# Performance work log

Measured on AMD Instinct MI355X. Metric: run time of the kernel, lower is better.

## Reference

```python
import jax, jax.numpy as jnp
import numpy as np

HEADS = 16
DIM_HEAD = 64
MASK_VALUE = -(np.finfo(np.float32).max / 2)


def setup_inputs() -> dict:
    key = jax.random.key(0)
    k1, k2, k3 = jax.random.split(key, 3)
    B, N, D = 2, 2048, 1024
    inner = HEADS * DIM_HEAD
    x = jax.random.normal(k1, (B, N, D), dtype=jnp.float32)
    w_qkv = jax.random.normal(k2, (D, 3 * inner), dtype=jnp.float32) * (D ** -0.5)
    w_out = jax.random.normal(k3, (inner, D), dtype=jnp.float32) * (inner ** -0.5)
    b_out = jnp.zeros((D,), dtype=jnp.float32)
    return {"x": x, "w_qkv": w_qkv, "w_out": w_out, "b_out": b_out}


def reference(x, w_qkv, w_out, b_out):
    B, N, D = x.shape
    H, Dh = HEADS, DIM_HEAD
    qkv = x @ w_qkv                                   # [B, N, 3*H*Dh]
    q, k, v = jnp.split(qkv, 3, axis=-1)
    # [B, N, H*Dh] -> [B, H, N, Dh]
    split_heads = lambda t: t.reshape(B, N, H, Dh).transpose(0, 2, 1, 3)
    q, k, v = split_heads(q), split_heads(k), split_heads(v)
    scale = Dh ** -0.5
    sim = jnp.einsum('bhid,bhjd->bhij', q, k) * scale  # [B, H, N, N]
    # causal additive mask: MASK_VALUE above the diagonal
    causal = jnp.triu(jnp.ones((N, N), dtype=bool), k=1)
    mask = jnp.where(causal, jnp.float32(MASK_VALUE), 0.0)
    sim = sim + mask[None, None, :, :]
    attn = jax.nn.softmax(sim, axis=-1)
    out = jnp.einsum('bhij,bhjd->bhid', attn, v)       # [B, H, N, Dh]
    out = out.transpose(0, 2, 1, 3).reshape(B, N, H * Dh)
    return out @ w_out + b_out
```

## Files before the change

kernel.cpp:

```cpp
#include <hip/hip_runtime.h>
#include <hip/hip_bf16.h>

typedef __attribute__((ext_vector_type(4)))  float    f32x4;
typedef __attribute__((ext_vector_type(16))) float    f32x16;
typedef __attribute__((ext_vector_type(8)))  short    bf16x8;
typedef __attribute__((ext_vector_type(4)))  short    s16x4;
typedef __attribute__((ext_vector_type(4)))  unsigned u32x4;

#define B_    2
#define N_    2048
#define D_    1024
#define HEADS 16
#define DH    64
#define M_    4096
#define INNER 1024

static __device__ __forceinline__ short f2bf(float f) {
    __hip_bfloat16 h = __float2bfloat16(f);
    return __builtin_bit_cast(short, h);
}
static __device__ __forceinline__ float bf2f(short s) {
    unsigned u = ((unsigned)(unsigned short)s) << 16;
    return __builtin_bit_cast(float, u);
}
static __device__ __forceinline__ unsigned pack2(float lo, float hi) {
    return ((unsigned)(unsigned short)f2bf(lo)) |
           (((unsigned)(unsigned short)f2bf(hi)) << 16);
}
static __device__ __forceinline__ unsigned cvtpk(float lo, float hi) {
    unsigned r;
    asm("v_cvt_pk_bf16_f32 %0, %1, %2" : "=v"(r) : "v"(lo), "v"(hi));
    return r;
}
static __device__ __forceinline__ void plswap(unsigned& a, unsigned& b) {
    asm("v_permlane32_swap_b32 %0, %1" : "+v"(a), "+v"(b));
}
static __device__ __forceinline__ float fexp2(float x) {
    float r;
    asm("v_exp_f32 %0, %1" : "=v"(r) : "v"(x));
    return r;
}
static __device__ __forceinline__ float flog2(float x) {
    float r;
    asm("v_log_f32 %0, %1" : "=v"(r) : "v"(x));
    return r;
}
static __device__ __forceinline__ float vmax16(f32x16 v) {
    float a = fmaxf(fmaxf(v[0], v[1]), fmaxf(v[2], v[3]));
    float b = fmaxf(fmaxf(v[4], v[5]), fmaxf(v[6], v[7]));
    float c = fmaxf(fmaxf(v[8], v[9]), fmaxf(v[10], v[11]));
    float d = fmaxf(fmaxf(v[12], v[13]), fmaxf(v[14], v[15]));
    return fmaxf(fmaxf(a, b), fmaxf(c, d));
}
static __device__ __forceinline__ float vsum16(f32x16 v) {
    float a = (v[0] + v[1]) + (v[2] + v[3]);
    float b = (v[4] + v[5]) + (v[6] + v[7]);
    float c = (v[8] + v[9]) + (v[10] + v[11]);
    float d = (v[12] + v[13]) + (v[14] + v[15]);
    return (a + b) + (c + d);
}

static __device__ __forceinline__ void transpose_tile(const float* __restrict__ in,
                                                      short* __restrict__ out,
                                                      int R, int C, int bx32, int by32,
                                                      float* t ) {
    int tx = threadIdx.x & 31, ty = threadIdx.x >> 5;
    int bx = bx32 * 32, by = by32 * 32;
#pragma unroll
    for (int j = 0; j < 32; j += 8)
        t[(ty + j) * 33 + tx] = in[(long)(by + ty + j) * C + bx + tx];
    __syncthreads();
#pragma unroll
    for (int j = 0; j < 32; j += 8)
        out[(long)(bx + ty + j) * R + by + tx] = f2bf(t[tx * 33 + ty + j]);
}

__global__ void __launch_bounds__(256) prep_k(const float* __restrict__ x,
                                              short* __restrict__ xb,
                                              const float* __restrict__ w_qkv,
                                              short* __restrict__ wqkvT,
                                              const float* __restrict__ w_out,
                                              short* __restrict__ woutT) {
    __shared__ float t[32 * 33];
    int bid = blockIdx.x;
    if (bid < 4096) {
        int i = bid * 256 + threadIdx.x;
        f32x4 v = ((const f32x4*)x)[i];
        s16x4 o;
        o[0] = f2bf(v[0]); o[1] = f2bf(v[1]); o[2] = f2bf(v[2]); o[3] = f2bf(v[3]);
        ((s16x4*)xb)[i] = o;
    } else if (bid < 4096 + 3072) {
        int tt = bid - 4096;
        transpose_tile(w_qkv, wqkvT, 1024, 3072, tt % 96, tt / 96, t);
    } else {
        int tt = bid - 7168;
        transpose_tile(w_out, woutT, 1024, 1024, tt % 32, tt / 32, t);
    }
}

template <int ROWS>
static __device__ __forceinline__ void stage_swz(const short* __restrict__ src,
                                                 int ldElems, short* lds, int tid) {
    constexpr int CH = (ROWS * 128) / (256 * 16);
#pragma unroll
    for (int c = 0; c < CH; ++c) {
        int o   = (tid + c * 256) * 16;
        int row = o >> 7;
        int kb  = (o & 127) ^ ((row & 7) << 4);
        const char* g = (const char*)src + (long)row * ldElems * 2 + kb;
        __builtin_amdgcn_global_load_lds(
            (const __attribute__((address_space(1))) void*)g,
            (__attribute__((address_space(3))) void*)((char*)lds + o), 16, 0, 0);
    }
}
static __device__ __forceinline__ bf16x8 lds_frag(const short* lds, int row, int kbyte) {
    return *(const bf16x8*)((const char*)lds + (row << 7) + (kbyte ^ ((row & 7) << 4)));
}

__global__ void __launch_bounds__(256) gemm_k(const short* __restrict__ A,
                                              const short* __restrict__ Bt, int K,
                                              short* __restrict__ q_out,
                                              short* __restrict__ k_out,
                                              short* __restrict__ v_out) {
    __shared__ __align__(16) short As[128 * 64];
    __shared__ __align__(16) short Bs[128 * 64];
    int tid = threadIdx.x;
    int lane = tid & 63, w = tid >> 6, wr = w >> 1, wc = w & 1;
    int l15 = lane & 15, lg = lane >> 4;
    int nx = gridDim.x;
    int flat = blockIdx.y * nx + blockIdx.x;
    int total = nx * gridDim.y;
    int cpx = total >> 3;
    int swz = (flat & 7) * cpx + (flat >> 3);
    int row0 = (swz / nx) * 128, col0 = (swz % nx) * 128;

    f32x4 acc[4][4] = {};

    for (int k0 = 0; k0 < K; k0 += 64) {
        stage_swz<128>(A + (long)row0 * K + k0, K, As, tid);
        stage_swz<128>(Bt + (long)col0 * K + k0, K, Bs, tid);
        __syncthreads();
#pragma unroll
        for (int kb = 0; kb < 2; ++kb) {
            int kbyte = kb * 64 + (lg << 4);
            bf16x8 af[4], bfr[4];
#pragma unroll
            for (int mr = 0; mr < 4; ++mr)
                af[mr] = lds_frag(As, wr * 64 + mr * 16 + l15, kbyte);
#pragma unroll
            for (int nr = 0; nr < 4; ++nr)
                bfr[nr] = lds_frag(Bs, wc * 64 + nr * 16 + l15, kbyte);
#pragma unroll
            for (int mr = 0; mr < 4; ++mr)
#pragma unroll
                for (int nr = 0; nr < 4; ++nr)
                    acc[mr][nr] = __builtin_amdgcn_mfma_f32_16x16x32_bf16(
                        af[mr], bfr[nr], acc[mr][nr], 0, 0, 0);
        }
        __syncthreads();
    }

#pragma unroll
    for (int mr = 0; mr < 4; ++mr)
#pragma unroll
        for (int nr = 0; nr < 4; ++nr) {
            int gr0 = row0 + wr * 64 + mr * 16 + (lg << 2);
            int gc  = col0 + wc * 64 + nr * 16 + l15;
            int which = gc >> 10, rem = gc & 1023;
            int h = rem >> 6, d = rem & 63;
            int b = gr0 >> 11, nn0 = gr0 & 2047;
            long bh32 = (long)(b * HEADS + h) * 32;
            if (which == 2) {
                int t = nn0 >> 6, ks = (nn0 >> 4) & 3, hb = (nn0 >> 3) & 1;
                long off = (((bh32 + t) * 2 + (d >> 5)) * 4 + ks) * 512
                           + ((hb << 5) + (d & 31)) * 8 + (nn0 & 4);
                s16x4 pk;
#pragma unroll
                for (int reg = 0; reg < 4; ++reg) pk[reg] = f2bf(acc[mr][nr][reg]);
                *(s16x4*)(v_out + off) = pk;
            } else if (which == 1) {
                int dk = d >> 4, hb = (d >> 3) & 1, j = d & 7;
                int t = nn0 >> 6, ss = (nn0 >> 5) & 1;
                long fbase = ((bh32 + t) * 2 + ss) * 4 + dk;
#pragma unroll
                for (int reg = 0; reg < 4; ++reg) {
                    int l31k = (nn0 + reg) & 31;
                    k_out[fbase * 512 + ((hb << 5) + l31k) * 8 + j] =
                        f2bf(acc[mr][nr][reg]);
                }
            } else {
                float sc = 0.180336880f;
#pragma unroll
                for (int reg = 0; reg < 4; ++reg) {
                    int gr = gr0 + reg;
                    int bb = gr >> 11, nn = gr & 2047;
                    q_out[((long)(bb * HEADS + h) * N_ + nn) * DH + d] =
                        f2bf(acc[mr][nr][reg] * sc);
                }
            }
        }
}

__global__ void __launch_bounds__(256) gemm2_k(const short* __restrict__ A,
                                               const short* __restrict__ Bt,
                                               float* __restrict__ f_out,
                                               const float* __restrict__ bias) {
    __shared__ __align__(16) short As[128 * 64];
    __shared__ __align__(16) short Bs[64 * 64];
    int tid = threadIdx.x;
    int lane = tid & 63, w = tid >> 6, wr = w >> 1, wc = w & 1;
    int l15 = lane & 15, lg = lane >> 4;
    const int K = 1024;
    int flat = blockIdx.y * 16 + blockIdx.x;
    int swz = (flat & 7) * 64 + (flat >> 3);
    int row0 = (swz >> 4) * 128, col0 = (swz & 15) * 64;

    f32x4 acc[4][2] = {};

    for (int k0 = 0; k0 < K; k0 += 64) {
        stage_swz<128>(A + (long)row0 * K + k0, K, As, tid);
        stage_swz<64>(Bt + (long)col0 * K + k0, K, Bs, tid);
        __syncthreads();
#pragma unroll
        for (int kb = 0; kb < 2; ++kb) {
            int kbyte = kb * 64 + (lg << 4);
            bf16x8 af[4], bfr[2];
#pragma unroll
            for (int mr = 0; mr < 4; ++mr)
                af[mr] = lds_frag(As, wr * 64 + mr * 16 + l15, kbyte);
#pragma unroll
            for (int nc = 0; nc < 2; ++nc)
                bfr[nc] = lds_frag(Bs, wc * 32 + nc * 16 + l15, kbyte);
#pragma unroll
            for (int mr = 0; mr < 4; ++mr)
#pragma unroll
                for (int nc = 0; nc < 2; ++nc)
                    acc[mr][nc] = __builtin_amdgcn_mfma_f32_16x16x32_bf16(
                        af[mr], bfr[nc], acc[mr][nc], 0, 0, 0);
        }
        __syncthreads();
    }

#pragma unroll
    for (int mr = 0; mr < 4; ++mr)
#pragma unroll
        for (int nc = 0; nc < 2; ++nc) {
            int gc = col0 + wc * 32 + nc * 16 + l15;
            float bv = bias[gc];
#pragma unroll
            for (int reg = 0; reg < 4; ++reg) {
                int gr = row0 + wr * 64 + mr * 16 + (lg << 2) + reg;
                f_out[(long)gr * D_ + gc] = acc[mr][nc][reg] + bv;
            }
        }
}

__global__ void __launch_bounds__(256, 2) attn_k(const short* __restrict__ Qb,
                                                 const short* __restrict__ Kf,
                                                 const short* __restrict__ Vf,
                                                 short* __restrict__ O0,
                                                 short* __restrict__ O1,
                                                 float* __restrict__ lse) {
    __shared__ __align__(16) short Ep[4][2048];
    int tid = threadIdx.x, lane = tid & 63, w = tid >> 6;
    int l31 = lane & 31, hbit = lane >> 5;
    int bq = blockIdx.x;
    int q4 = bq >> 8, rest = bq & 255;
    int bh = rest >> 3, p = rest & 7;
    int x = (q4 < 2) ? (15 - p) : p;
    int seg = q4 & 1;
    int t0 = seg ? (x + 1) : 0;
    int t1 = seg ? (2 * x + 2) : (x + 1);

    const short* Qh = Qb + (long)bh * N_ * DH;
    const short* Kh = Kf + (long)bh * 32 * 4096;
    const short* Vh = Vf + (long)bh * 32 * 4096;
    int lofs = lane * 8;

    int q0 = x * 128 + w * 32;
    int qg = q0 + l31;
    int t1w = min(t1, ((q0 + 31) >> 6) + 1);

    bf16x8 qf[4];
#pragma unroll
    for (int kf = 0; kf < 4; ++kf)
        qf[kf] = *(const bf16x8*)(Qh + (long)qg * DH + kf * 16 + hbit * 8);

    f32x16 o[2] = {};
    float m = -1e30f, l = 0.f;

    for (int t = t0; t < t1w; ++t) {
        const short* kb = Kh + (long)t * 4096;
        const short* vb = Vh + (long)t * 4096;
        int khb = t * 64;

        bf16x8 kfr[2][4];
#pragma unroll
        for (int ss = 0; ss < 2; ++ss)
#pragma unroll
            for (int dk = 0; dk < 4; ++dk)
                kfr[ss][dk] = *(const bf16x8*)(kb + (ss * 4 + dk) * 512 + lofs);

        f32x16 S[2] = {};
        __builtin_amdgcn_s_setprio(1);
#pragma unroll
        for (int ss = 0; ss < 2; ++ss)
#pragma unroll
            for (int dk = 0; dk < 4; ++dk)
                S[ss] = __builtin_amdgcn_mfma_f32_32x32x16_bf16(
                    kfr[ss][dk], qf[dk], S[ss], 0, 0, 0);
        __builtin_amdgcn_s_setprio(0);

        bf16x8 vf[2][4];
#pragma unroll
        for (int df = 0; df < 2; ++df)
#pragma unroll
            for (int ks = 0; ks < 4; ++ks)
                vf[df][ks] = *(const bf16x8*)(vb + (df * 4 + ks) * 512 + lofs);

        if (khb + 63 > q0) {
            int kvl = khb + 4 * hbit;
#pragma unroll
            for (int ss = 0; ss < 2; ++ss)
#pragma unroll
                for (int r = 0; r < 16; ++r) {
                    int kv = kvl + 32 * ss + (r & 3) + 8 * (r >> 2);
                    if (kv > qg) S[ss][r] = -1e30f;
                }
        }

        float pm = fmaxf(vmax16(S[0]), vmax16(S[1]));
        pm = fmaxf(pm, __shfl_xor(pm, 32));
        if (!__all(pm <= m + 8.0f)) {
            float mn = fmaxf(m, pm);
            float corr = fexp2(m - mn);
            m = mn;
            l *= corr;
#pragma unroll
            for (int df = 0; df < 2; ++df)
#pragma unroll
                for (int r = 0; r < 16; ++r) o[df][r] *= corr;
        }
#pragma unroll
        for (int ss = 0; ss < 2; ++ss)
#pragma unroll
            for (int r = 0; r < 16; ++r)
                S[ss][r] = fexp2(S[ss][r] - m);
        l += vsum16(S[0]) + vsum16(S[1]);

        __builtin_amdgcn_s_setprio(1);
#pragma unroll
        for (int ss = 0; ss < 2; ++ss) {
#pragma unroll
            for (int hs = 0; hs < 2; ++hs) {
                unsigned w0 = cvtpk(S[ss][hs * 8 + 0], S[ss][hs * 8 + 1]);
                unsigned w1 = cvtpk(S[ss][hs * 8 + 2], S[ss][hs * 8 + 3]);
                unsigned w2 = cvtpk(S[ss][hs * 8 + 4], S[ss][hs * 8 + 5]);
                unsigned w3 = cvtpk(S[ss][hs * 8 + 6], S[ss][hs * 8 + 7]);
                plswap(w0, w2);
                plswap(w1, w3);
                bf16x8 pfrag = __builtin_bit_cast(bf16x8, (u32x4){w0, w1, w2, w3});
                int ks = ss * 2 + hs;
#pragma unroll
                for (int df = 0; df < 2; ++df)
                    o[df] = __builtin_amdgcn_mfma_f32_32x32x16_bf16(
                        vf[df][ks], pfrag, o[df], 0, 0, 0);
            }
        }
        __builtin_amdgcn_s_setprio(0);
    }

    l += __shfl_xor(l, 32);
    float linv = (l > 0.f) ? 1.0f / l : 0.f;
    if (hbit == 0)
        lse[seg * (32 * N_) + bh * N_ + qg] =
            (l > 0.f) ? (m + flog2(l)) : -__builtin_inff();

    char* Epw = (char*)&Ep[w][0];
#pragma unroll
    for (int df = 0; df < 2; ++df)
#pragma unroll
        for (int r = 0; r < 16; r += 2) {
            unsigned pk = pack2(o[df][r] * linv, o[df][r + 1] * linv);
            int d = df * 32 + (r & 3) + 8 * (r >> 2) + 4 * hbit;
            int cb = d * 2;
            *(unsigned*)(Epw + (l31 << 7) + (cb ^ ((l31 & 7) << 4))) = pk;
        }
    __syncthreads();

    int b = bh >> 4, h = bh & 15;
    int lr = lane >> 1, lc = lane & 1;
    const char* rbase = Epw + (lr << 7);
    long orow = seg ? ((long)(bh * N_ + q0 + lr)) * 64 + lc * 32
                    : ((long)(b * N_ + q0 + lr)) * INNER + h * DH + lc * 32;
    short* dst = seg ? O1 : O0;
#pragma unroll
    for (int j = 0; j < 4; ++j) {
        int cb = lc * 64 + j * 16;
        bf16x8 vv = *(const bf16x8*)(rbase + (cb ^ ((lr & 7) << 4)));
        *(bf16x8*)(dst + orow + j * 8) = vv;
    }
}

__global__ void __launch_bounds__(256) merge_k(short* __restrict__ Ab,
                                               const short* __restrict__ O1,
                                               const float* __restrict__ lse) {
    int gid = blockIdx.x * 256 + threadIdx.x;
    int row = gid >> 3, d0 = (gid & 7) * 8;
    int bh = row >> 11, n = row & 2047;
    float l0 = lse[row];
    float l1 = lse[32 * N_ + row];
    float Mx = fmaxf(l0, l1);
    float w0 = fexp2(l0 - Mx), w1 = fexp2(l1 - Mx);
    float inv = 1.0f / (w0 + w1);
    w0 *= inv; w1 *= inv;
    int b = bh >> 4, h = bh & 15;
    long a_off = ((long)(b * N_ + n) * HEADS + h) * DH + d0;
    long o_off = (long)row * DH + d0;
    bf16x8 v0 = *(const bf16x8*)(Ab + a_off);
    bf16x8 v1 = *(const bf16x8*)(O1 + o_off);
    bf16x8 r;
#pragma unroll
    for (int i = 0; i < 8; ++i)
        r[i] = f2bf(w0 * bf2f(v0[i]) + w1 * bf2f(v1[i]));
    *(bf16x8*)(Ab + a_off) = r;
}


extern "C" void kernel_launch(void* const* d_in, const int* in_sizes, int n_in,
                              void* d_out, int out_size, void* d_ws, size_t ws_size,
                              hipStream_t stream) {
    const float* x     = (const float*)d_in[0];
    const float* w_qkv = (const float*)d_in[1];
    const float* w_out = (const float*)d_in[2];
    const float* b_out = (const float*)d_in[3];
    float* out = (float*)d_out;

    char* ws = (char*)d_ws;
    const size_t MB = 1024 * 1024;
    short* xb    = (short*)(ws + 0 * MB);
    short* wqkvT = (short*)(ws + 8 * MB);
    short* woutT = (short*)(ws + 14 * MB);
    short* Qb    = (short*)(ws + 16 * MB);
    short* Kfb   = (short*)(ws + 24 * MB);
    short* Vfb   = (short*)(ws + 32 * MB);
    short* Ab    = (short*)(ws + 40 * MB);
    short* O1    = (short*)(ws + 0 * MB);
    float* lse   = (float*)(ws + 8 * MB);

    prep_k<<<dim3(4096 + 3072 + 1024), 256, 0, stream>>>(
        x, xb, w_qkv, wqkvT, w_out, woutT);

    gemm_k<<<dim3(3072 / 128, M_ / 128), 256, 0, stream>>>(
        xb, wqkvT, 1024, Qb, Kfb, Vfb);

    attn_k<<<dim3(1024), 256, 0, stream>>>(Qb, Kfb, Vfb, Ab, O1, lse);
    merge_k<<<dim3((32 * N_ * 8) / 256), 256, 0, stream>>>(Ab, O1, lse);

    gemm2_k<<<dim3(1024 / 64, M_ / 128), 256, 0, stream>>>(Ab, woutT, out, b_out);
}
```

Measured before the change: 101.9 us.

## Process 128-key tiles per iteration with per-wave diagonal trimming in attention

The attention loop now walks 128-key tiles instead of 64-key tiles, which halves the number of iterations and softmax/rescale rounds. On the diagonal tile each wave only loads and computes the 32-key sub-blocks it needs (w+1 of them), and the split-KV segments are redefined in terms of the larger tiles. Sched barriers separate the K and V load phases. The cost is more live registers for K/V fragments and S under the 2-blocks-per-CU launch bound, which may cause spills or lower occupancy.

```diff
diff --git a/kernel.cpp b/kernel.cpp
--- a/kernel.cpp
+++ b/kernel.cpp
@@ -269,8 +269,9 @@
     int bh = rest >> 3, p = rest & 7;
     int x = (q4 < 2) ? (15 - p) : p;
     int seg = q4 & 1;
-    int t0 = seg ? (x + 1) : 0;
-    int t1 = seg ? (2 * x + 2) : (x + 1);
+    int sdiv = (x + 2) >> 1;
+    int tA = seg ? sdiv : 0;
+    int tB = seg ? (x + 1) : sdiv;
 
     const short* Qh = Qb + (long)bh * N_ * DH;
     const short* Kh = Kf + (long)bh * 32 * 4096;
@@ -279,7 +280,6 @@
 
     int q0 = x * 128 + w * 32;
     int qg = q0 + l31;
-    int t1w = min(t1, ((q0 + 31) >> 6) + 1);
 
     bf16x8 qf[4];
 #pragma unroll
@@ -287,49 +287,62 @@
         qf[kf] = *(const bf16x8*)(Qh + (long)qg * DH + kf * 16 + hbit * 8);
 
     f32x16 o[2] = {};
+    const f32x16 Zv = {};
     float m = -1e30f, l = 0.f;
 
-    for (int t = t0; t < t1w; ++t) {
-        const short* kb = Kh + (long)t * 4096;
-        const short* vb = Vh + (long)t * 4096;
-        int khb = t * 64;
-
-        bf16x8 kfr[2][4];
-#pragma unroll
-        for (int ss = 0; ss < 2; ++ss)
-#pragma unroll
-            for (int dk = 0; dk < 4; ++dk)
-                kfr[ss][dk] = *(const bf16x8*)(kb + (ss * 4 + dk) * 512 + lofs);
-
-        f32x16 S[2] = {};
+#define VS(df, s16) kv[((df) << 1) + ((s16) >> 2)][(s16) & 3]
+
+    for (int t = tA; t < tB; ++t) {
+        const short* kb = Kh + (long)t * 8192;
+        const short* vb = Vh + (long)t * 8192;
+        bool diag = (t == x);
+        int nss = diag ? (w + 1) : 4;
+
+        bf16x8 kv[4][4];
+#pragma unroll
+        for (int ss = 0; ss < 4; ++ss)
+            if (ss < nss)
+#pragma unroll
+                for (int dk = 0; dk < 4; ++dk)
+                    kv[ss][dk] = *(const bf16x8*)(kb + ss * 2048 + dk * 512 + lofs);
+
+        f32x16 S[4];
         __builtin_amdgcn_s_setprio(1);
 #pragma unroll
-        for (int ss = 0; ss < 2; ++ss)
-#pragma unroll
-            for (int dk = 0; dk < 4; ++dk)
-                S[ss] = __builtin_amdgcn_mfma_f32_32x32x16_bf16(
-                    kfr[ss][dk], qf[dk], S[ss], 0, 0, 0);
+        for (int ss = 0; ss < 4; ++ss)
+            if (ss < nss) {
+                S[ss] = Zv;
+#pragma unroll
+                for (int dk = 0; dk < 4; ++dk)
+                    S[ss] = __builtin_amdgcn_mfma_f32_32x32x16_bf16(
+                        kv[ss][dk], qf[dk], S[ss], 0, 0, 0);
+            }
         __builtin_amdgcn_s_setprio(0);
-
-        bf16x8 vf[2][4];
-#pragma unroll
-        for (int df = 0; df < 2; ++df)
-#pragma unroll
-            for (int ks = 0; ks < 4; ++ks)
-                vf[df][ks] = *(const bf16x8*)(vb + (df * 4 + ks) * 512 + lofs);
-
-        if (khb + 63 > q0) {
-            int kvl = khb + 4 * hbit;
-#pragma unroll
-            for (int ss = 0; ss < 2; ++ss)
-#pragma unroll
-                for (int r = 0; r < 16; ++r) {
-                    int kv = kvl + 32 * ss + (r & 3) + 8 * (r >> 2);
-                    if (kv > qg) S[ss][r] = -1e30f;
-                }
-        }
-
-        float pm = fmaxf(vmax16(S[0]), vmax16(S[1]));
+        __builtin_amdgcn_sched_barrier(0);
+
+#pragma unroll
+        for (int s16 = 0; s16 < 8; ++s16)
+            if (s16 < 2 * nss)
+#pragma unroll
+                for (int df = 0; df < 2; ++df)
+                    VS(df, s16) = *(const bf16x8*)(vb + (s16 >> 2) * 4096 +
+                                                   df * 2048 + (s16 & 3) * 512 + lofs);
+        __builtin_amdgcn_sched_barrier(0);
+
+        if (diag) {
+#pragma unroll
+            for (int ss = 0; ss < 4; ++ss)
+                if (ss == w)
+#pragma unroll
+                    for (int r = 0; r < 16; ++r)
+                        if (4 * hbit + (r & 3) + 8 * (r >> 2) > l31)
+                            S[ss][r] = -1e30f;
+        }
+
+        float pm = -1e30f;
+#pragma unroll
+        for (int ss = 0; ss < 4; ++ss)
+            if (ss < nss) pm = fmaxf(pm, vmax16(S[ss]));
         pm = fmaxf(pm, __shfl_xor(pm, 32));
         if (!__all(pm <= m + 8.0f)) {
             float mn = fmaxf(m, pm);
@@ -341,34 +354,37 @@
 #pragma unroll
                 for (int r = 0; r < 16; ++r) o[df][r] *= corr;
         }
-#pragma unroll
-        for (int ss = 0; ss < 2; ++ss)
-#pragma unroll
-            for (int r = 0; r < 16; ++r)
-                S[ss][r] = fexp2(S[ss][r] - m);
-        l += vsum16(S[0]) + vsum16(S[1]);
+        float ts = 0.f;
+#pragma unroll
+        for (int ss = 0; ss < 4; ++ss)
+            if (ss < nss) {
+#pragma unroll
+                for (int r = 0; r < 16; ++r)
+                    S[ss][r] = fexp2(S[ss][r] - m);
+                ts += vsum16(S[ss]);
+            }
+        l += ts;
 
         __builtin_amdgcn_s_setprio(1);
 #pragma unroll
-        for (int ss = 0; ss < 2; ++ss) {
-#pragma unroll
-            for (int hs = 0; hs < 2; ++hs) {
-                unsigned w0 = cvtpk(S[ss][hs * 8 + 0], S[ss][hs * 8 + 1]);
-                unsigned w1 = cvtpk(S[ss][hs * 8 + 2], S[ss][hs * 8 + 3]);
-                unsigned w2 = cvtpk(S[ss][hs * 8 + 4], S[ss][hs * 8 + 5]);
-                unsigned w3 = cvtpk(S[ss][hs * 8 + 6], S[ss][hs * 8 + 7]);
+        for (int s16 = 0; s16 < 8; ++s16)
+            if (s16 < 2 * nss) {
+                const int sp = s16 >> 1, hs = s16 & 1;
+                unsigned w0 = cvtpk(S[sp][hs * 8 + 0], S[sp][hs * 8 + 1]);
+                unsigned w1 = cvtpk(S[sp][hs * 8 + 2], S[sp][hs * 8 + 3]);
+                unsigned w2 = cvtpk(S[sp][hs * 8 + 4], S[sp][hs * 8 + 5]);
+                unsigned w3 = cvtpk(S[sp][hs * 8 + 6], S[sp][hs * 8 + 7]);
                 plswap(w0, w2);
                 plswap(w1, w3);
                 bf16x8 pfrag = __builtin_bit_cast(bf16x8, (u32x4){w0, w1, w2, w3});
-                int ks = ss * 2 + hs;
 #pragma unroll
                 for (int df = 0; df < 2; ++df)
                     o[df] = __builtin_amdgcn_mfma_f32_32x32x16_bf16(
-                        vf[df][ks], pfrag, o[df], 0, 0, 0);
+                        VS(df, s16), pfrag, o[df], 0, 0, 0);
             }
-        }
         __builtin_amdgcn_s_setprio(0);
     }
+#undef VS
 
     l += __shfl_xor(l, 32);
     float linv = (l > 0.f) ? 1.0f / l : 0.f;
```

Result: slower. 108.0 us (+6.0%).
